# Kernel optimization log

Hardware: AMD Instinct MI355X
Metric: run time of the kernel (lower is better)

## Reference

```python
import jax, jax.numpy as jnp
import numpy as np

B = 131072   # batch of state samples
H = 512      # hidden width of reconstructed subnets
EPS_DIAG = 0.1  # diagonal regularization ensuring M is invertible


def setup_inputs() -> dict:
    key = jax.random.key(0)
    ks = jax.random.split(key, 20)
    f32 = jnp.float32
    inp = {
        "q":      jax.random.normal(ks[0], (B, 3), dtype=f32),
        "q_dot":  jax.random.normal(ks[1], (B, 3), dtype=f32),
        "s":      jax.random.normal(ks[2], (B, 3), dtype=f32),
        "s_Ddot": jax.random.normal(ks[3], (B, 3), dtype=f32),
        "tau":    jax.random.normal(ks[4], (B, 3), dtype=f32),
        # viscous / coulomb friction coefficients (f_v1..3, f_c1..3)
        "fv": jnp.full((3,), 0.05, dtype=f32),
        "fc": jnp.full((3,), 0.05, dtype=f32),
        # Mass net: 3 -> H -> 9
        "W1m": jax.random.normal(ks[5], (3, H), dtype=f32) * 0.1,
        "b1m": jnp.zeros((H,), dtype=f32),
        "W2m": jax.random.normal(ks[6], (H, 9), dtype=f32) * 0.05,
        "b2m": jnp.zeros((9,), dtype=f32),
        # Gravity net: 3 -> H -> 3
        "W1g": jax.random.normal(ks[7], (3, H), dtype=f32) * 0.1,
        "b1g": jnp.zeros((H,), dtype=f32),
        "W2g": jax.random.normal(ks[8], (H, 3), dtype=f32) * 0.05,
        "b2g": jnp.zeros((3,), dtype=f32),
        # KAB net: concat(q, s, s_Ddot)=9 -> H -> 3
        "W1k": jax.random.normal(ks[9], (9, H), dtype=f32) * 0.1,
        "b1k": jnp.zeros((H,), dtype=f32),
        "W2k": jax.random.normal(ks[10], (H, 3), dtype=f32) * 0.05,
        "b2k": jnp.zeros((3,), dtype=f32),
    }
    return inp


def reference(q, q_dot, s, s_Ddot, tau, fv, fc,
              W1m, b1m, W2m, b2m,
              W1g, b1g, W2g, b2g,
              W1k, b1k, W2k, b2k) -> jnp.ndarray:
    # Mass matrix net -> [B,3,3], made SPD-ish so inv(M) is well defined
    hm = jnp.tanh(q @ W1m + b1m)                       # [B,H]
    Mraw = (hm @ W2m + b2m).reshape(-1, 3, 3)          # [B,3,3]
    M = jnp.einsum('bij,bkj->bik', Mraw, Mraw) + EPS_DIAG * jnp.eye(3, dtype=q.dtype)

    # Gravity net -> [B,3]
    hg = jnp.tanh(q @ W1g + b1g)
    G = hg @ W2g + b2g

    # KAB net on concat(q, s, s_Ddot) -> [B,3]
    x = jnp.concatenate([q, s, s_Ddot], axis=-1)       # [B,9]
    hk = jnp.tanh(x @ W1k + b1k)
    KAB = hk @ W2k + b2k

    # diag(fv) @ q_dot and diag(fc) @ sign(q_dot) are elementwise scalings
    rhs = -G + KAB - fv * q_dot - fc * jnp.sign(q_dot) + tau  # [B,3]

    # q_Ddot = inv(M) @ rhs  (solve is the same math, fewer ops)
    q_Ddot = jnp.linalg.solve(M, rhs[..., None]).squeeze(-1)  # [B,3]
    return q_Ddot
```

## Files before the change

### kernel.cpp

```cpp
#include <hip/hip_runtime.h>
#include <math.h>

#define HDIM 512
#define NCH1 96
#define NCH2 48
#define EPS_DIAG 0.1f

typedef __fp16 h2 __attribute__((ext_vector_type(2)));
typedef __fp16 h4 __attribute__((ext_vector_type(4)));
typedef __fp16 h8 __attribute__((ext_vector_type(8)));
typedef float f32x4 __attribute__((ext_vector_type(4)));
typedef unsigned int u32x4 __attribute__((ext_vector_type(4)));

__device__ __forceinline__ u32x4 tanh_pack4(
    float x0, float y0, float x1, float y1,
    float x2, float y2, float x3, float y3,
    unsigned int c3u, unsigned int c2u, unsigned int c1u, unsigned int c0u)
{
    unsigned int t0, t1, t2, t3, u0, u1, u2, u3, p0, p1, p2, p3;
    asm("v_cvt_pkrtz_f16_f32 %[t0], %[x0], %[y0]\n\t"
        "v_cvt_pkrtz_f16_f32 %[t1], %[x1], %[y1]\n\t"
        "v_cvt_pkrtz_f16_f32 %[t2], %[x2], %[y2]\n\t"
        "v_cvt_pkrtz_f16_f32 %[t3], %[x3], %[y3]\n\t"
        "v_pk_mul_f16 %[u0], %[t0], %[t0]\n\t"
        "v_pk_mul_f16 %[u1], %[t1], %[t1]\n\t"
        "v_pk_mul_f16 %[u2], %[t2], %[t2]\n\t"
        "v_pk_mul_f16 %[u3], %[t3], %[t3]\n\t"
        "v_pk_fma_f16 %[p0], %[c3], %[u0], %[c2]\n\t"
        "v_pk_fma_f16 %[p1], %[c3], %[u1], %[c2]\n\t"
        "v_pk_fma_f16 %[p2], %[c3], %[u2], %[c2]\n\t"
        "v_pk_fma_f16 %[p3], %[c3], %[u3], %[c2]\n\t"
        "v_pk_fma_f16 %[p0], %[p0], %[u0], %[c1]\n\t"
        "v_pk_fma_f16 %[p1], %[p1], %[u1], %[c1]\n\t"
        "v_pk_fma_f16 %[p2], %[p2], %[u2], %[c1]\n\t"
        "v_pk_fma_f16 %[p3], %[p3], %[u3], %[c1]\n\t"
        "v_pk_fma_f16 %[p0], %[p0], %[u0], %[c0]\n\t"
        "v_pk_fma_f16 %[p1], %[p1], %[u1], %[c0]\n\t"
        "v_pk_fma_f16 %[p2], %[p2], %[u2], %[c0]\n\t"
        "v_pk_fma_f16 %[p3], %[p3], %[u3], %[c0]\n\t"
        "v_pk_mul_f16 %[t0], %[t0], %[p0]\n\t"
        "v_pk_mul_f16 %[t1], %[t1], %[p1]\n\t"
        "v_pk_mul_f16 %[t2], %[t2], %[p2]\n\t"
        "v_pk_mul_f16 %[t3], %[t3], %[p3]"
        : [t0]"=&v"(t0), [t1]"=&v"(t1), [t2]"=&v"(t2), [t3]"=&v"(t3),
          [u0]"=&v"(u0), [u1]"=&v"(u1), [u2]"=&v"(u2), [u3]"=&v"(u3),
          [p0]"=&v"(p0), [p1]"=&v"(p1), [p2]"=&v"(p2), [p3]"=&v"(p3)
        : [x0]"v"(x0), [y0]"v"(y0), [x1]"v"(x1), [y1]"v"(y1),
          [x2]"v"(x2), [y2]"v"(y2), [x3]"v"(x3), [y3]"v"(y3),
          [c3]"v"(c3u), [c2]"v"(c2u), [c1]"v"(c1u), [c0]"v"(c0u));
    u32x4 r;
    r[0] = t0; r[1] = t1; r[2] = t2; r[3] = t3;
    return r;
}

__device__ __forceinline__ float w1c_at(int k, int hid,
    const float* W1m, const float* b1m, const float* W1g, const float* b1g,
    const float* W1k, const float* b1k)
{
    if (hid < 512)  { if (k < 3) return W1m[k*HDIM + hid]; if (k == 9) return b1m[hid]; return 0.f; }
    if (hid < 1024) { const int h = hid - 512;
                      if (k < 3) return W1g[k*HDIM + h];  if (k == 9) return b1g[h];  return 0.f; }
    const int h = hid - 1024;
    if (k < 9) return W1k[k*HDIM + h]; if (k == 9) return b1k[h]; return 0.f;
}

__global__ void pack_frags(const float* __restrict__ W1m, const float* __restrict__ b1m,
                           const float* __restrict__ W2m,
                           const float* __restrict__ W1g, const float* __restrict__ b1g,
                           const float* __restrict__ W2g,
                           const float* __restrict__ W1k, const float* __restrict__ b1k,
                           const float* __restrict__ W2k,
                           __fp16* __restrict__ frag)
{
    const int tid = blockIdx.x * blockDim.x + threadIdx.x;
    if (tid >= (NCH1 + NCH2) * 64) return;
    const int c = tid >> 6, l = tid & 63;
    const int m = l & 15, kq = l >> 4;
    if (c < NCH1) {
        __fp16* dst = frag + (size_t)tid * 4;
        const int t = c >> 1, phase = c & 1;
        const int hid = 32*t + 8*(m >> 2) + (m & 3) + 4*phase;
        #pragma unroll
        for (int j = 0; j < 4; ++j) {
            const int k = kq*4 + j;
            dst[j] = (__fp16)((k < 10) ? w1c_at(k, hid, W1m, b1m, W1g, b1g, W1k, b1k) : 0.f);
        }
    } else {
        __fp16* dst = frag + (size_t)NCH1 * 64 * 4 + (size_t)(tid - NCH1 * 64) * 8;
        const int t = c - NCH1;
        #pragma unroll
        for (int j = 0; j < 8; ++j) {
            const int hid = 32*t + kq*8 + j;
            float v = 0.f;
            if (hid < 512)       { if (m < 9)             v = W2m[hid*9 + m]; }
            else if (hid < 1024) { if (m >= 9 && m < 12)  v = W2g[(hid-512)*3 + (m-9)]; }
            else                 { if (m >= 12 && m < 15) v = W2k[(hid-1024)*3 + (m-12)]; }
            dst[j] = (__fp16)v;
        }
    }
}

__device__ __forceinline__ h4 make_ax4(const float* __restrict__ q,
                                       const float* __restrict__ s,
                                       const float* __restrict__ s_Ddot,
                                       int sm, int quad)
{
    const float q0 = q[3*sm+0], q1 = q[3*sm+1], q2 = q[3*sm+2];
    const float s0 = s[3*sm+0], s1 = s[3*sm+1], s2 = s[3*sm+2];
    const float d0 = s_Ddot[3*sm+0], d1 = s_Ddot[3*sm+1], d2 = s_Ddot[3*sm+2];
    const bool z0 = (quad == 0), z1 = (quad == 1), z2 = (quad == 2);
    h4 ax;
    ax[0] = (__fp16)(z0 ? q0 : (z1 ? s1 : (z2 ? d2  : 0.f)));
    ax[1] = (__fp16)(z0 ? q1 : (z1 ? s2 : (z2 ? 1.f : 0.f)));
    ax[2] = (__fp16)(z0 ? q2 : (z1 ? d0 : 0.f));
    ax[3] = (__fp16)(z0 ? s0 : (z1 ? d1 : 0.f));
    return ax;
}

__global__ __launch_bounds__(256, 4) void dyn_kernel(
    const __fp16* __restrict__ frag,
    const float* __restrict__ q, const float* __restrict__ q_dot,
    const float* __restrict__ s, const float* __restrict__ s_Ddot,
    const float* __restrict__ tau,
    const float* __restrict__ fv, const float* __restrict__ fc,
    const float* __restrict__ b2m, const float* __restrict__ b2g,
    const float* __restrict__ b2k,
    float* __restrict__ out, int n)
{
    __shared__ float ebuf[4][64][20];

    const int lane = threadIdx.x & 63;
    const int w    = threadIdx.x >> 6;
    const int col  = lane & 15;
    const int quad = lane >> 4;
    const int th   = w & 1;
    const int base64 = (blockIdx.x * 2 + (w >> 1)) * 64;

    int sm0 = base64 +  0 + col; if (sm0 >= n) sm0 = n - 1;
    int sm1 = base64 + 16 + col; if (sm1 >= n) sm1 = n - 1;
    int sm2 = base64 + 32 + col; if (sm2 >= n) sm2 = n - 1;
    int sm3 = base64 + 48 + col; if (sm3 >= n) sm3 = n - 1;
    const h4 ax0 = make_ax4(q, s, s_Ddot, sm0, quad);
    const h4 ax1 = make_ax4(q, s, s_Ddot, sm1, quad);
    const h4 ax2 = make_ax4(q, s, s_Ddot, sm2, quad);
    const h4 ax3 = make_ax4(q, s, s_Ddot, sm3, quad);

    const h2 C0h = {(__fp16)0.993654f,    (__fp16)0.993654f};
    const h2 C1h = {(__fp16)-0.29463f,    (__fp16)-0.29463f};
    const h2 C2h = {(__fp16)0.0695331f,   (__fp16)0.0695331f};
    const h2 C3h = {(__fp16)-0.00696328f, (__fp16)-0.00696328f};
    const unsigned int c0u = __builtin_bit_cast(unsigned int, C0h);
    const unsigned int c1u = __builtin_bit_cast(unsigned int, C1h);
    const unsigned int c2u = __builtin_bit_cast(unsigned int, C2h);
    const unsigned int c3u = __builtin_bit_cast(unsigned int, C3h);

    const f32x4 zero4 = {0.f, 0.f, 0.f, 0.f};
    f32x4 acc0 = zero4, acc1 = zero4, acc2 = zero4, acc3 = zero4;

    const h4* p1 = (const h4*)frag + (size_t)(48 * th) * 64 + lane;
    const h8* p2 = (const h8*)(frag + (size_t)NCH1 * 64 * 4) + (size_t)(24 * th) * 64 + lane;

#define T4(PA, PB) tanh_pack4((PA)[0], (PA)[1], (PA)[2], (PA)[3],             \
                              (PB)[0], (PB)[1], (PB)[2], (PB)[3],             \
                              c3u, c2u, c1u, c0u)

#define BODY(W1A, W1B, W2V) do {                                              \
        __builtin_amdgcn_s_setprio(1);                                        \
        f32x4 pa0 = __builtin_amdgcn_mfma_f32_16x16x16f16((W1A), ax0, zero4, 0, 0, 0); \
        f32x4 pb0 = __builtin_amdgcn_mfma_f32_16x16x16f16((W1B), ax0, zero4, 0, 0, 0); \
        f32x4 pa1 = __builtin_amdgcn_mfma_f32_16x16x16f16((W1A), ax1, zero4, 0, 0, 0); \
        f32x4 pb1 = __builtin_amdgcn_mfma_f32_16x16x16f16((W1B), ax1, zero4, 0, 0, 0); \
        f32x4 pa2 = __builtin_amdgcn_mfma_f32_16x16x16f16((W1A), ax2, zero4, 0, 0, 0); \
        f32x4 pb2 = __builtin_amdgcn_mfma_f32_16x16x16f16((W1B), ax2, zero4, 0, 0, 0); \
        f32x4 pa3 = __builtin_amdgcn_mfma_f32_16x16x16f16((W1A), ax3, zero4, 0, 0, 0); \
        f32x4 pb3 = __builtin_amdgcn_mfma_f32_16x16x16f16((W1B), ax3, zero4, 0, 0, 0); \
        __builtin_amdgcn_s_setprio(0);                                        \
        __builtin_amdgcn_sched_group_barrier(0x8, 8, 0);   \
        u32x4 uv0 = T4(pa0, pb0);                                             \
        u32x4 uv1 = T4(pa1, pb1);                                             \
        acc0 = __builtin_amdgcn_mfma_f32_16x16x32_f16((W2V), __builtin_bit_cast(h8, uv0), acc0, 0, 0, 0); \
        u32x4 uv2 = T4(pa2, pb2);                                             \
        acc1 = __builtin_amdgcn_mfma_f32_16x16x32_f16((W2V), __builtin_bit_cast(h8, uv1), acc1, 0, 0, 0); \
        u32x4 uv3 = T4(pa3, pb3);                                             \
        acc2 = __builtin_amdgcn_mfma_f32_16x16x32_f16((W2V), __builtin_bit_cast(h8, uv2), acc2, 0, 0, 0); \
        acc3 = __builtin_amdgcn_mfma_f32_16x16x32_f16((W2V), __builtin_bit_cast(h8, uv3), acc3, 0, 0, 0); \
    } while (0)

    h4 a0 = p1[0],   b0 = p1[64];
    h4 a1 = p1[128], b1 = p1[192];
    h8 c0 = p2[0],   c1 = p2[64];
    int t = 0;
    for (; t < 24 - 4; t += 2) {
        p1 += 256; p2 += 128;
        h4 na0 = p1[0],   nb0 = p1[64];
        h4 na1 = p1[128], nb1 = p1[192];
        h8 nc0 = p2[0],   nc1 = p2[64];
        BODY(a0, b0, c0);
        BODY(a1, b1, c1);
        a0 = na0; b0 = nb0; c0 = nc0;
        a1 = na1; b1 = nb1; c1 = nc1;
    }
    {
        p1 += 256; p2 += 128;
        h4 na0 = p1[0],   nb0 = p1[64];
        h4 na1 = p1[128], nb1 = p1[192];
        h8 nc0 = p2[0],   nc1 = p2[64];
        BODY(a0, b0, c0);
        BODY(a1, b1, c1);
        BODY(na0, nb0, nc0);
        BODY(na1, nb1, nc1);
    }
#undef BODY
#undef T4

    *(f32x4*)(&ebuf[w][ 0 + col][4*quad]) = acc0;
    *(f32x4*)(&ebuf[w][16 + col][4*quad]) = acc1;
    *(f32x4*)(&ebuf[w][32 + col][4*quad]) = acc2;
    *(f32x4*)(&ebuf[w][48 + col][4*quad]) = acc3;
    __syncthreads();

    if (th == 0) {
        const int i = base64 + lane;
        if (i < n) {
            const float* Ra = ebuf[w][lane];
            const float* Rb = ebuf[w + 1][lane];
            float R[15];
            #pragma unroll
            for (int j = 0; j < 15; ++j) R[j] = Ra[j] + Rb[j];

            const float bM0 = R[0]  + b2m[0], bM1 = R[1]  + b2m[1], bM2 = R[2]  + b2m[2];
            const float bM3 = R[3]  + b2m[3], bM4 = R[4]  + b2m[4], bM5 = R[5]  + b2m[5];
            const float bM6 = R[6]  + b2m[6], bM7 = R[7]  + b2m[7], bM8 = R[8]  + b2m[8];
            const float bG0 = R[9]  + b2g[0], bG1 = R[10] + b2g[1], bG2 = R[11] + b2g[2];
            const float bK0 = R[12] + b2k[0], bK1 = R[13] + b2k[1], bK2 = R[14] + b2k[2];

            const float m00 = bM0*bM0 + bM1*bM1 + bM2*bM2 + EPS_DIAG;
            const float m01 = bM0*bM3 + bM1*bM4 + bM2*bM5;
            const float m02 = bM0*bM6 + bM1*bM7 + bM2*bM8;
            const float m11 = bM3*bM3 + bM4*bM4 + bM5*bM5 + EPS_DIAG;
            const float m12 = bM3*bM6 + bM4*bM7 + bM5*bM8;
            const float m22 = bM6*bM6 + bM7*bM7 + bM8*bM8 + EPS_DIAG;

            const float qd0 = q_dot[3*i+0], qd1 = q_dot[3*i+1], qd2 = q_dot[3*i+2];
            const float t0 = tau[3*i+0], t1 = tau[3*i+1], t2 = tau[3*i+2];
            const float fv0 = fv[0], fv1 = fv[1], fv2 = fv[2];
            const float fc0 = fc[0], fc1 = fc[1], fc2 = fc[2];
            const float sg0 = (qd0 > 0.f) ? 1.f : ((qd0 < 0.f) ? -1.f : 0.f);
            const float sg1 = (qd1 > 0.f) ? 1.f : ((qd1 < 0.f) ? -1.f : 0.f);
            const float sg2 = (qd2 > 0.f) ? 1.f : ((qd2 < 0.f) ? -1.f : 0.f);
            const float r0 = -bG0 + bK0 - fv0*qd0 - fc0*sg0 + t0;
            const float r1 = -bG1 + bK1 - fv1*qd1 - fc1*sg1 + t1;
            const float r2 = -bG2 + bK2 - fv2*qd2 - fc2*sg2 + t2;

            const float c00 = m11*m22 - m12*m12;
            const float c01 = m02*m12 - m01*m22;
            const float c02 = m01*m12 - m02*m11;
            const float det = m00*c00 + m01*c01 + m02*c02;
            const float idet = 1.0f / det;
            const float i11 = m00*m22 - m02*m02;
            const float i12 = m01*m02 - m00*m12;
            const float i22 = m00*m11 - m01*m01;

            out[3*i+0] = (c00*r0 + c01*r1 + c02*r2) * idet;
            out[3*i+1] = (c01*r0 + i11*r1 + i12*r2) * idet;
            out[3*i+2] = (c02*r0 + i12*r1 + i22*r2) * idet;
        }
    }
}

extern "C" void kernel_launch(void* const* d_in, const int* in_sizes, int n_in,
                              void* d_out, int out_size, void* d_ws, size_t ws_size,
                              hipStream_t stream) {
    const float* q      = (const float*)d_in[0];
    const float* q_dot  = (const float*)d_in[1];
    const float* s      = (const float*)d_in[2];
    const float* s_Ddot = (const float*)d_in[3];
    const float* tau    = (const float*)d_in[4];
    const float* fv     = (const float*)d_in[5];
    const float* fc     = (const float*)d_in[6];
    const float* W1m    = (const float*)d_in[7];
    const float* b1m    = (const float*)d_in[8];
    const float* W2m    = (const float*)d_in[9];
    const float* b2m    = (const float*)d_in[10];
    const float* W1g    = (const float*)d_in[11];
    const float* b1g    = (const float*)d_in[12];
    const float* W2g    = (const float*)d_in[13];
    const float* b2g    = (const float*)d_in[14];
    const float* W1k    = (const float*)d_in[15];
    const float* b1k    = (const float*)d_in[16];
    const float* W2k    = (const float*)d_in[17];
    const float* b2k    = (const float*)d_in[18];
    float* out = (float*)d_out;
    __fp16* frag = (__fp16*)d_ws;

    const int n = in_sizes[0] / 3;

    pack_frags<<<((NCH1 + NCH2) * 64 + 255) / 256, 256, 0, stream>>>(
        W1m, b1m, W2m, W1g, b1g, W2g, W1k, b1k, W2k, frag);

    const int blocks = (n + 127) / 128;
    dyn_kernel<<<blocks, 256, 0, stream>>>(frag, q, q_dot, s, s_Ddot, tau, fv, fc,
                                           b2m, b2g, b2k, out, n);
}
```

Baseline: 125.1 us.

## Halve per-wave sample tile to 32 and raise occupancy target to 8 blocks

Each wave now processes 32 samples (two 16-column MFMA tiles) instead of 64, halving accumulators and W1 products held in registers, and launch bounds raise the occupancy target. Tanh polynomial constants are passed as scalar registers to save VGPRs, and the prefetch loop is simplified to one chunk per iteration. The cost is that every weight fragment is reloaded from memory twice as often per sample, and the grid has twice as many blocks.

```diff
diff --git a/kernel.cpp b/kernel.cpp
--- a/kernel.cpp
+++ b/kernel.cpp
@@ -15,7 +15,7 @@
 __device__ __forceinline__ u32x4 tanh_pack4(
     float x0, float y0, float x1, float y1,
     float x2, float y2, float x3, float y3,
-    unsigned int c3u, unsigned int c2u, unsigned int c1u, unsigned int c0u)
+    unsigned int c3s, unsigned int c2v, unsigned int c1s, unsigned int c0s)
 {
     unsigned int t0, t1, t2, t3, u0, u1, u2, u3, p0, p1, p2, p3;
     asm("v_cvt_pkrtz_f16_f32 %[t0], %[x0], %[y0]\n\t"
@@ -47,7 +47,7 @@
           [p0]"=&v"(p0), [p1]"=&v"(p1), [p2]"=&v"(p2), [p3]"=&v"(p3)
         : [x0]"v"(x0), [y0]"v"(y0), [x1]"v"(x1), [y1]"v"(y1),
           [x2]"v"(x2), [y2]"v"(y2), [x3]"v"(x3), [y3]"v"(y3),
-          [c3]"v"(c3u), [c2]"v"(c2u), [c1]"v"(c1u), [c0]"v"(c0u));
+          [c3]"s"(c3s), [c2]"v"(c2v), [c1]"s"(c1s), [c0]"s"(c0s));
     u32x4 r;
     r[0] = t0; r[1] = t1; r[2] = t2; r[3] = t3;
     return r;
@@ -117,7 +117,7 @@
     return ax;
 }
 
-__global__ __launch_bounds__(256, 4) void dyn_kernel(
+__global__ __launch_bounds__(256, 8) void dyn_kernel(
     const __fp16* __restrict__ frag,
     const float* __restrict__ q, const float* __restrict__ q_dot,
     const float* __restrict__ s, const float* __restrict__ s_Ddot,
@@ -127,23 +127,19 @@
     const float* __restrict__ b2k,
     float* __restrict__ out, int n)
 {
-    __shared__ float ebuf[4][64][20];
+    __shared__ float ebuf[4][32][20];
 
     const int lane = threadIdx.x & 63;
     const int w    = threadIdx.x >> 6;
     const int col  = lane & 15;
     const int quad = lane >> 4;
     const int th   = w & 1;
-    const int base64 = (blockIdx.x * 2 + (w >> 1)) * 64;
-
-    int sm0 = base64 +  0 + col; if (sm0 >= n) sm0 = n - 1;
-    int sm1 = base64 + 16 + col; if (sm1 >= n) sm1 = n - 1;
-    int sm2 = base64 + 32 + col; if (sm2 >= n) sm2 = n - 1;
-    int sm3 = base64 + 48 + col; if (sm3 >= n) sm3 = n - 1;
+    const int base32 = (blockIdx.x * 2 + (w >> 1)) * 32;
+
+    int sm0 = base32 +  0 + col; if (sm0 >= n) sm0 = n - 1;
+    int sm1 = base32 + 16 + col; if (sm1 >= n) sm1 = n - 1;
     const h4 ax0 = make_ax4(q, s, s_Ddot, sm0, quad);
     const h4 ax1 = make_ax4(q, s, s_Ddot, sm1, quad);
-    const h4 ax2 = make_ax4(q, s, s_Ddot, sm2, quad);
-    const h4 ax3 = make_ax4(q, s, s_Ddot, sm3, quad);
 
     const h2 C0h = {(__fp16)0.993654f,    (__fp16)0.993654f};
     const h2 C1h = {(__fp16)-0.29463f,    (__fp16)-0.29463f};
@@ -155,7 +151,7 @@
     const unsigned int c3u = __builtin_bit_cast(unsigned int, C3h);
 
     const f32x4 zero4 = {0.f, 0.f, 0.f, 0.f};
-    f32x4 acc0 = zero4, acc1 = zero4, acc2 = zero4, acc3 = zero4;
+    f32x4 acc0 = zero4, acc1 = zero4;
 
     const h4* p1 = (const h4*)frag + (size_t)(48 * th) * 64 + lane;
     const h8* p2 = (const h8*)(frag + (size_t)NCH1 * 64 * 4) + (size_t)(24 * th) * 64 + lane;
@@ -170,57 +166,33 @@
         f32x4 pb0 = __builtin_amdgcn_mfma_f32_16x16x16f16((W1B), ax0, zero4, 0, 0, 0); \
         f32x4 pa1 = __builtin_amdgcn_mfma_f32_16x16x16f16((W1A), ax1, zero4, 0, 0, 0); \
         f32x4 pb1 = __builtin_amdgcn_mfma_f32_16x16x16f16((W1B), ax1, zero4, 0, 0, 0); \
-        f32x4 pa2 = __builtin_amdgcn_mfma_f32_16x16x16f16((W1A), ax2, zero4, 0, 0, 0); \
-        f32x4 pb2 = __builtin_amdgcn_mfma_f32_16x16x16f16((W1B), ax2, zero4, 0, 0, 0); \
-        f32x4 pa3 = __builtin_amdgcn_mfma_f32_16x16x16f16((W1A), ax3, zero4, 0, 0, 0); \
-        f32x4 pb3 = __builtin_amdgcn_mfma_f32_16x16x16f16((W1B), ax3, zero4, 0, 0, 0); \
         __builtin_amdgcn_s_setprio(0);                                        \
-        __builtin_amdgcn_sched_group_barrier(0x8, 8, 0);   \
+        __builtin_amdgcn_sched_group_barrier(0x8, 4, 0);   \
         u32x4 uv0 = T4(pa0, pb0);                                             \
         u32x4 uv1 = T4(pa1, pb1);                                             \
         acc0 = __builtin_amdgcn_mfma_f32_16x16x32_f16((W2V), __builtin_bit_cast(h8, uv0), acc0, 0, 0, 0); \
-        u32x4 uv2 = T4(pa2, pb2);                                             \
         acc1 = __builtin_amdgcn_mfma_f32_16x16x32_f16((W2V), __builtin_bit_cast(h8, uv1), acc1, 0, 0, 0); \
-        u32x4 uv3 = T4(pa3, pb3);                                             \
-        acc2 = __builtin_amdgcn_mfma_f32_16x16x32_f16((W2V), __builtin_bit_cast(h8, uv2), acc2, 0, 0, 0); \
-        acc3 = __builtin_amdgcn_mfma_f32_16x16x32_f16((W2V), __builtin_bit_cast(h8, uv3), acc3, 0, 0, 0); \
     } while (0)
 
-    h4 a0 = p1[0],   b0 = p1[64];
-    h4 a1 = p1[128], b1 = p1[192];
-    h8 c0 = p2[0],   c1 = p2[64];
-    int t = 0;
-    for (; t < 24 - 4; t += 2) {
-        p1 += 256; p2 += 128;
-        h4 na0 = p1[0],   nb0 = p1[64];
-        h4 na1 = p1[128], nb1 = p1[192];
-        h8 nc0 = p2[0],   nc1 = p2[64];
+    h4 a0 = p1[0], b0 = p1[64];
+    h8 c0 = p2[0];
+    for (int t = 0; t < 24 - 1; ++t) {
+        p1 += 128; p2 += 64;
+        h4 a1 = p1[0], b1 = p1[64];
+        h8 c1 = p2[0];
         BODY(a0, b0, c0);
-        BODY(a1, b1, c1);
-        a0 = na0; b0 = nb0; c0 = nc0;
-        a1 = na1; b1 = nb1; c1 = nc1;
+        a0 = a1; b0 = b1; c0 = c1;
     }
-    {
-        p1 += 256; p2 += 128;
-        h4 na0 = p1[0],   nb0 = p1[64];
-        h4 na1 = p1[128], nb1 = p1[192];
-        h8 nc0 = p2[0],   nc1 = p2[64];
-        BODY(a0, b0, c0);
-        BODY(a1, b1, c1);
-        BODY(na0, nb0, nc0);
-        BODY(na1, nb1, nc1);
-    }
+    BODY(a0, b0, c0);
 #undef BODY
 #undef T4
 
     *(f32x4*)(&ebuf[w][ 0 + col][4*quad]) = acc0;
     *(f32x4*)(&ebuf[w][16 + col][4*quad]) = acc1;
-    *(f32x4*)(&ebuf[w][32 + col][4*quad]) = acc2;
-    *(f32x4*)(&ebuf[w][48 + col][4*quad]) = acc3;
     __syncthreads();
 
-    if (th == 0) {
-        const int i = base64 + lane;
+    if (th == 0 && lane < 32) {
+        const int i = base32 + lane;
         if (i < n) {
             const float* Ra = ebuf[w][lane];
             const float* Rb = ebuf[w + 1][lane];
@@ -298,7 +270,7 @@
     pack_frags<<<((NCH1 + NCH2) * 64 + 255) / 256, 256, 0, stream>>>(
         W1m, b1m, W2m, W1g, b1g, W2g, W1k, b1k, W2k, frag);
 
-    const int blocks = (n + 127) / 128;
+    const int blocks = (n + 63) / 64;
     dyn_kernel<<<blocks, 256, 0, stream>>>(frag, q, q_dot, s, s_Ddot, tau, fv, fc,
                                            b2m, b2g, b2k, out, n);
 }
```

New measurement: 124.4 us. Within noise of the previous version (-0.6%).
